# Kernel tuning notes

Hardware: AMD Instinct MI355X
Metric: run time of the kernel (lower is better)

The kernel has to match this reference:

```python
import jax, jax.numpy as jnp
import numpy as np

N, M = 2048, 256
INPUT_DIM, EMBED_DIM, HIDDEN = 512, 256, 512


def setup_inputs() -> dict:
    key = jax.random.key(0)
    ks = jax.random.split(key, 12)
    s = 0.02
    inp = {
        "x": jax.random.normal(ks[0], (N, INPUT_DIM), dtype=jnp.float32),
        "tuples": jax.random.randint(ks[1], (M, 3), 0, 8, dtype=jnp.int64),
        # x_net: Linear(input_dim, hidden) -> ReLU -> Linear(hidden, embed_dim) -> ReLU
        "Wa": s * jax.random.normal(ks[2], (HIDDEN, INPUT_DIM), dtype=jnp.float32),
        "ba": jnp.zeros((HIDDEN,), dtype=jnp.float32),
        "Wb": s * jax.random.normal(ks[3], (EMBED_DIM, HIDDEN), dtype=jnp.float32),
        "bb": jnp.zeros((EMBED_DIM,), dtype=jnp.float32),
        # embedding tables
        "E_pred": s * jax.random.normal(ks[4], (8, EMBED_DIM), dtype=jnp.float32),
        "E_filt": s * jax.random.normal(ks[5], (192, EMBED_DIM), dtype=jnp.float32),
        "E_reo": s * jax.random.normal(ks[6], (8, EMBED_DIM), dtype=jnp.float32),
        # mlp: Linear(2*embed_dim, hidden) -> ReLU -> Linear(hidden, 1)
        "W1": s * jax.random.normal(ks[7], (HIDDEN, 2 * EMBED_DIM), dtype=jnp.float32),
        "b1": jnp.zeros((HIDDEN,), dtype=jnp.float32),
        "W2": s * jax.random.normal(ks[8], (1, HIDDEN), dtype=jnp.float32),
        "b2": jnp.zeros((1,), dtype=jnp.float32),
    }
    return inp


def reference(x, tuples, Wa, ba, Wb, bb, E_pred, E_filt, E_reo, W1, b1, W2, b2):
    # x_net: two Linear+ReLU layers -> x_emb [N, D]
    h_x = jax.nn.relu(jnp.einsum('ni,hi->nh', x, Wa) + ba)
    x_emb = jax.nn.relu(jnp.einsum('nh,dh->nd', h_x, Wb) + bb)
    # tuple embedding sum -> t_emb [M, D]
    t_emb = E_pred[tuples[:, 0]] + E_filt[tuples[:, 1]] + E_reo[tuples[:, 2]]
    # mlp first layer on concat([x_exp, t_exp]) == Wx @ x_emb + Wt @ t_emb (split W1)
    D = x_emb.shape[1]
    W1x, W1t = W1[:, :D], W1[:, D:]
    hx = jnp.einsum('nd,hd->nh', x_emb, W1x)          # [N, H]
    ht = jnp.einsum('md,hd->mh', t_emb, W1t)          # [M, H]
    h = jax.nn.relu(hx[:, None, :] + ht[None, :, :] + b1)  # [N, M, H]
    out = jnp.einsum('nmh,h->nm', h, W2[0]) + b2[0]   # [N, M]
    return out
```

## Files before the change

kernel.cpp:

```cpp
#include <hip/hip_runtime.h>

constexpr int N_     = 2048;
constexpr int IN_DIM = 512;
constexpr int HID    = 512;
constexpr int EMB    = 256;
constexpr int M_     = 256;

typedef __attribute__((ext_vector_type(8))) short short8;
typedef __attribute__((ext_vector_type(4))) float f32x4;
typedef __attribute__((ext_vector_type(2))) _Float16 h2v;

union U32H2 { unsigned int u; h2v v; };

__device__ __forceinline__ unsigned short f2bf(float f) {
    union { float f; unsigned int u; } v; v.f = f;
    return (unsigned short)((v.u + 0x7fffu + ((v.u >> 16) & 1u)) >> 16);
}
__device__ __forceinline__ unsigned int packh2(float a, float b) {
    U32H2 r; r.v[0] = (_Float16)a; r.v[1] = (_Float16)b; return r.u;
}
__device__ __forceinline__ h2v relu2(h2v s) {
#if defined(__has_builtin) && __has_builtin(__builtin_elementwise_max)
    U32H2 z; z.u = 0u;
    return __builtin_elementwise_max(s, z.v);
#else
    U32H2 t; t.v = s;
    const unsigned int m = ((t.u & 0x80000000u) ? 0xFFFF0000u : 0u) |
                           ((t.u & 0x00008000u) ? 0x0000FFFFu : 0u);
    t.u &= ~m;
    return t.v;
#endif
}

__global__ __launch_bounds__(256)
void prep(const float* __restrict__ x, const float* __restrict__ Wa,
          const float* __restrict__ Wb, const float* __restrict__ W1,
          const int* __restrict__ tuples, const float* __restrict__ Ep,
          const float* __restrict__ Ef, const float* __restrict__ Er,
          const float* __restrict__ w2,
          unsigned short* __restrict__ x_bf, unsigned short* __restrict__ Wa_bf,
          unsigned short* __restrict__ Wb_bf, unsigned short* __restrict__ W1x_bf,
          unsigned short* __restrict__ W1t_bf, unsigned short* __restrict__ t_emb_bf,
          unsigned int* __restrict__ w2p)
{
    const int b = blockIdx.x, t = threadIdx.x;
    if (b < 1664) {
        int q = b * 256 + t;
        float4 v; ushort4 u;
        if (q < 262144) {
            v = ((const float4*)x)[q];
            u.x = f2bf(v.x); u.y = f2bf(v.y); u.z = f2bf(v.z); u.w = f2bf(v.w);
            ((ushort4*)x_bf)[q] = u;
        } else if ((q -= 262144) < 65536) {
            v = ((const float4*)Wa)[q];
            u.x = f2bf(v.x); u.y = f2bf(v.y); u.z = f2bf(v.z); u.w = f2bf(v.w);
            ((ushort4*)Wa_bf)[q] = u;
        } else if ((q -= 65536) < 32768) {
            v = ((const float4*)Wb)[q];
            u.x = f2bf(v.x); u.y = f2bf(v.y); u.z = f2bf(v.z); u.w = f2bf(v.w);
            ((ushort4*)Wb_bf)[q] = u;
        } else {
            q -= 32768;
            v = ((const float4*)W1)[q];
            u.x = f2bf(v.x); u.y = f2bf(v.y); u.z = f2bf(v.z); u.w = f2bf(v.w);
            const int row = q >> 7, c = (q & 127) * 4;
            if (c < 256) ((ushort4*)W1x_bf)[(row * 256 + c) >> 2] = u;
            else         ((ushort4*)W1t_bf)[(row * 256 + c - 256) >> 2] = u;
        }
    } else if (b < 1728) {
        const int idx = (b - 1664) * 256 + t;
        const int m = idx >> 6, q = idx & 63;
        const int t0 = tuples[m * 3 + 0];
        const int t1 = tuples[m * 3 + 1];
        const int t2 = tuples[m * 3 + 2];
        const float4 a = ((const float4*)(Ep + t0 * EMB))[q];
        const float4 c = ((const float4*)(Ef + t1 * EMB))[q];
        const float4 d = ((const float4*)(Er + t2 * EMB))[q];
        ushort4 u;
        u.x = f2bf(a.x + c.x + d.x);
        u.y = f2bf(a.y + c.y + d.y);
        u.z = f2bf(a.z + c.z + d.z);
        u.w = f2bf(a.w + c.w + d.w);
        ((ushort4*)t_emb_bf)[m * 64 + q] = u;
    } else {
        w2p[t] = packh2(w2[2 * t], w2[2 * t + 1]);
    }
}

template<int BM, int BN, bool RELU, bool BIASC>
__global__ __launch_bounds__(256)
void gemm_bf16(const unsigned short* __restrict__ A, int lda,
               const unsigned short* __restrict__ W, int ldw,
               const float* __restrict__ bias,
               unsigned short* __restrict__ Cout, int ldc, int K)
{
    constexpr int BK = 64;
    constexpr int SM = BM / 2, SN = BN / 2;
    constexpr int FM = SM / 16, FN = SN / 16;
    constexpr int AIT = BM / 32, WIT = BN / 32;
    __shared__ unsigned short As[BM][BK + 8];
    __shared__ unsigned short Bs[BN][BK + 8];

    const int tid  = threadIdx.x;
    const int row0 = blockIdx.x * BM, col0 = blockIdx.y * BN;
    const int wv = tid >> 6, lane = tid & 63;
    const int wr = wv >> 1, wc = wv & 1;
    const int lr = lane & 15, lq = lane >> 4;

    f32x4 acc[FM][FN];
#pragma unroll
    for (int i = 0; i < FM; ++i)
#pragma unroll
        for (int j = 0; j < FN; ++j) acc[i][j] = (f32x4)0.f;

    short8 pa[AIT], pw[WIT];
    auto issue = [&](int k0) {
#pragma unroll
        for (int i = 0; i < AIT; ++i) {
            const int idx = tid + i * 256, r = idx >> 3, c8 = idx & 7;
            pa[i] = *(const short8*)&A[(size_t)(row0 + r) * lda + k0 + c8 * 8];
        }
#pragma unroll
        for (int i = 0; i < WIT; ++i) {
            const int idx = tid + i * 256, r = idx >> 3, c8 = idx & 7;
            pw[i] = *(const short8*)&W[(size_t)(col0 + r) * ldw + k0 + c8 * 8];
        }
    };
    auto store = [&]() {
#pragma unroll
        for (int i = 0; i < AIT; ++i) {
            const int idx = tid + i * 256, r = idx >> 3, c8 = idx & 7;
            *(short8*)&As[r][c8 * 8] = pa[i];
        }
#pragma unroll
        for (int i = 0; i < WIT; ++i) {
            const int idx = tid + i * 256, r = idx >> 3, c8 = idx & 7;
            *(short8*)&Bs[r][c8 * 8] = pw[i];
        }
    };

    issue(0); store();
    const int NC = K / BK;
    for (int c = 0; c < NC; ++c) {
        if (c + 1 < NC) issue((c + 1) * BK);
        __syncthreads();
#pragma unroll
        for (int ks = 0; ks < 2; ++ks) {
            short8 af[FM], bfr[FN];
#pragma unroll
            for (int i = 0; i < FM; ++i)
                af[i] = *(const short8*)&As[wr * SM + i * 16 + lr][ks * 32 + lq * 8];
#pragma unroll
            for (int j = 0; j < FN; ++j)
                bfr[j] = *(const short8*)&Bs[wc * SN + j * 16 + lr][ks * 32 + lq * 8];
#pragma unroll
            for (int i = 0; i < FM; ++i)
#pragma unroll
                for (int j = 0; j < FN; ++j)
                    acc[i][j] = __builtin_amdgcn_mfma_f32_16x16x32_bf16(
                        af[i], bfr[j], acc[i][j], 0, 0, 0);
        }
        __syncthreads();
        if (c + 1 < NC) store();
    }

#pragma unroll
    for (int i = 0; i < FM; ++i) {
#pragma unroll
        for (int j = 0; j < FN; ++j) {
            const int colb = col0 + wc * SN + j * 16 + lr;
#pragma unroll
            for (int e = 0; e < 4; ++e) {
                const int row = row0 + wr * SM + i * 16 + lq * 4 + e;
                float v = acc[i][j][e];
                if (BIASC) v += bias[colb];
                if (RELU)  v = fmaxf(v, 0.f);
                Cout[(size_t)row * ldc + colb] = f2bf(v);
            }
        }
    }
}

__global__ __launch_bounds__(256)
void gemm_pair(const unsigned short* __restrict__ W1x_bf,
               const unsigned short* __restrict__ W1t_bf,
               const unsigned short* __restrict__ x_emb_bf,
               const unsigned short* __restrict__ t_emb_bf,
               const float* __restrict__ b1,
               unsigned int* __restrict__ hxT_p,
               unsigned int* __restrict__ cmT_p)
{
    constexpr int BM = 32, BN = 64, BK = 64;
    constexpr int SM = 16, SN = 32, FN = 2;
    __shared__ unsigned short As[BM][BK + 8];
    __shared__ unsigned short Bs[BN][BK + 8];

    const unsigned short* A; const unsigned short* B;
    const float* bias; unsigned int* outp; int ldc, col0;
    if (blockIdx.y < 32) {
        A = W1x_bf; B = x_emb_bf; bias = nullptr; outp = hxT_p;
        ldc = N_; col0 = blockIdx.y * BN;
    } else {
        A = W1t_bf; B = t_emb_bf; bias = b1; outp = cmT_p;
        ldc = M_; col0 = (blockIdx.y - 32) * BN;
    }
    const int K = EMB, row0 = blockIdx.x * BM;

    const int tid = threadIdx.x;
    const int wv = tid >> 6, lane = tid & 63;
    const int wr = wv >> 1, wc = wv & 1;
    const int lr = lane & 15, lq = lane >> 4;

    f32x4 acc[FN];
#pragma unroll
    for (int j = 0; j < FN; ++j) acc[j] = (f32x4)0.f;

    short8 pa, pw[2];
    auto issue = [&](int k0) {
        { const int r = tid >> 3, c8 = tid & 7;
          pa = *(const short8*)&A[(size_t)(row0 + r) * K + k0 + c8 * 8]; }
#pragma unroll
        for (int i = 0; i < 2; ++i) {
            const int idx = tid + i * 256, r = idx >> 3, c8 = idx & 7;
            pw[i] = *(const short8*)&B[(size_t)(col0 + r) * K + k0 + c8 * 8];
        }
    };
    auto store = [&]() {
        { const int r = tid >> 3, c8 = tid & 7;
          *(short8*)&As[r][c8 * 8] = pa; }
#pragma unroll
        for (int i = 0; i < 2; ++i) {
            const int idx = tid + i * 256, r = idx >> 3, c8 = idx & 7;
            *(short8*)&Bs[r][c8 * 8] = pw[i];
        }
    };

    issue(0); store();
    const int NC = K / BK;
    for (int c = 0; c < NC; ++c) {
        if (c + 1 < NC) issue((c + 1) * BK);
        __syncthreads();
#pragma unroll
        for (int ks = 0; ks < 2; ++ks) {
            short8 af, bfr[FN];
            af = *(const short8*)&As[wr * SM + lr][ks * 32 + lq * 8];
#pragma unroll
            for (int j = 0; j < FN; ++j)
                bfr[j] = *(const short8*)&Bs[wc * SN + j * 16 + lr][ks * 32 + lq * 8];
#pragma unroll
            for (int j = 0; j < FN; ++j)
                acc[j] = __builtin_amdgcn_mfma_f32_16x16x32_bf16(
                    af, bfr[j], acc[j], 0, 0, 0);
        }
        __syncthreads();
        if (c + 1 < NC) store();
    }

    const int rowb = row0 + wr * SM + lq * 4;
#pragma unroll
    for (int j = 0; j < FN; ++j) {
        const int colb = col0 + wc * SN + j * 16 + lr;
#pragma unroll
        for (int e2 = 0; e2 < 2; ++e2) {
            float v0 = acc[j][2 * e2], v1 = acc[j][2 * e2 + 1];
            if (bias) { v0 += bias[rowb + 2 * e2]; v1 += bias[rowb + 2 * e2 + 1]; }
            outp[(size_t)((rowb >> 1) + e2) * ldc + colb] = packh2(v0, v1);
        }
    }
}

__global__ __launch_bounds__(256, 4)
void fused_out(const unsigned int* __restrict__ hxT_p,
               const unsigned int* __restrict__ cmT_p,
               const unsigned int* __restrict__ w2p,
               unsigned int* __restrict__ part_u32)
{
    constexpr int TN = 64, TM = 32, H2B = 64;
    __shared__ unsigned int Hs[H2B][TN + 4];
    __shared__ unsigned int Cs[H2B][TM + 4];
    __shared__ unsigned int Wsh[H2B];

    const int tid = threadIdx.x;
    const int tx = tid & 15, ty = tid >> 4;
    const int n0 = blockIdx.x * TN;
    const int m0 = blockIdx.y * TM;
    const int z  = blockIdx.z;
    const int kb = z * H2B;

#pragma unroll
    for (int p = 0; p < 4; ++p) {
        const int idx = tid + p * 256, r = idx >> 4, c4 = idx & 15;
        *(uint4*)&Hs[r][c4 * 4] =
            *(const uint4*)&hxT_p[(size_t)(kb + r) * N_ + n0 + c4 * 4];
    }
#pragma unroll
    for (int p = 0; p < 2; ++p) {
        const int idx = tid + p * 256, r = idx >> 3, c4 = idx & 7;
        *(uint4*)&Cs[r][c4 * 4] =
            *(const uint4*)&cmT_p[(size_t)(kb + r) * M_ + m0 + c4 * 4];
    }
    if (tid < H2B) Wsh[tid] = w2p[kb + tid];
    __syncthreads();

    float accf[4][2];
    U32H2 facc[4][2];
#pragma unroll
    for (int i = 0; i < 4; ++i)
#pragma unroll
        for (int j = 0; j < 2; ++j) { accf[i][j] = 0.f; facc[i][j].u = 0u; }

#pragma unroll
    for (int hb = 0; hb < H2B / 8; ++hb) {
#pragma unroll
        for (int hh = 0; hh < 8; ++hh) {
            const int h = hb * 8 + hh;
            const uint4 av = *(const uint4*)&Hs[h][ty * 4];
            const uint2 bv = *(const uint2*)&Cs[h][tx * 2];
            U32H2 w; w.u = Wsh[h];
            U32H2 a[4], b[2];
            a[0].u = av.x; a[1].u = av.y; a[2].u = av.z; a[3].u = av.w;
            b[0].u = bv.x; b[1].u = bv.y;
#pragma unroll
            for (int i = 0; i < 4; ++i) {
#pragma unroll
                for (int j = 0; j < 2; ++j) {
                    const h2v s = relu2(a[i].v + b[j].v);
                    facc[i][j].v = s * w.v + facc[i][j].v;
                }
            }
        }
#pragma unroll
        for (int i = 0; i < 4; ++i)
#pragma unroll
            for (int j = 0; j < 2; ++j) {
                accf[i][j] += (float)facc[i][j].v[0] + (float)facc[i][j].v[1];
                facc[i][j].u = 0u;
            }
    }

#pragma unroll
    for (int i = 0; i < 4; ++i) {
        const int n = n0 + ty * 4 + i;
        part_u32[((size_t)z * N_ + n) * (M_ / 2) + (m0 >> 1) + tx] =
            packh2(accf[i][0], accf[i][1]);
    }
}

__global__ __launch_bounds__(256)
void reduce_out(const unsigned short* __restrict__ part,
                const float* __restrict__ b2,
                float* __restrict__ out)
{
    const int g = blockIdx.x * 256 + threadIdx.x;
    const int n = g >> 5;
    const int m0 = (g & 31) * 8;
    const float bb = b2[0];
    float s[8];
#pragma unroll
    for (int i = 0; i < 8; ++i) s[i] = bb;
#pragma unroll
    for (int zz = 0; zz < 4; ++zz) {
        const uint4 v = *(const uint4*)&part[((size_t)zz * N_ + n) * M_ + m0];
        const unsigned int vv[4] = {v.x, v.y, v.z, v.w};
#pragma unroll
        for (int q = 0; q < 4; ++q) {
            U32H2 u; u.u = vv[q];
            s[2 * q]     += (float)u.v[0];
            s[2 * q + 1] += (float)u.v[1];
        }
    }
    float4 o0 = {s[0], s[1], s[2], s[3]};
    float4 o1 = {s[4], s[5], s[6], s[7]};
    *(float4*)&out[(size_t)n * M_ + m0]     = o0;
    *(float4*)&out[(size_t)n * M_ + m0 + 4] = o1;
}

extern "C" void kernel_launch(void* const* d_in, const int* in_sizes, int n_in,
                              void* d_out, int out_size, void* d_ws, size_t ws_size,
                              hipStream_t stream)
{
    const float* x      = (const float*)d_in[0];
    const int*   tuples = (const int*)d_in[1];
    const float* Wa     = (const float*)d_in[2];
    const float* ba     = (const float*)d_in[3];
    const float* Wb     = (const float*)d_in[4];
    const float* bb     = (const float*)d_in[5];
    const float* E_pred = (const float*)d_in[6];
    const float* E_filt = (const float*)d_in[7];
    const float* E_reo  = (const float*)d_in[8];
    const float* W1     = (const float*)d_in[9];
    const float* b1     = (const float*)d_in[10];
    const float* W2     = (const float*)d_in[11];
    const float* b2     = (const float*)d_in[12];
    float* out = (float*)d_out;

    char* w = (char*)d_ws;
    unsigned short* x_bf     = (unsigned short*)(w + 0);
    unsigned int*   hxT_p    = (unsigned int*)(w + 0);
    unsigned short* h_x_bf   = (unsigned short*)(w + 2097152);
    unsigned int*   part_u32 = (unsigned int*)(w + 2097152);
    unsigned short* x_emb_bf = (unsigned short*)(w + 4194304);
    unsigned short* Wa_bf    = (unsigned short*)(w + 5242880);
    unsigned short* Wb_bf    = (unsigned short*)(w + 5767168);
    unsigned short* W1x_bf   = (unsigned short*)(w + 6029312);
    unsigned int*   cmT_p    = (unsigned int*)(w + 6291456);
    unsigned short* W1t_bf   = (unsigned short*)(w + 6553600);
    unsigned short* t_emb_bf = (unsigned short*)(w + 6815744);
    unsigned int*   w2p      = (unsigned int*)(w + 6946816);

    prep<<<dim3(1729), dim3(256), 0, stream>>>(
        x, Wa, Wb, W1, tuples, E_pred, E_filt, E_reo, W2,
        x_bf, Wa_bf, Wb_bf, W1x_bf, W1t_bf, t_emb_bf, w2p);

    gemm_bf16<32, 64, true, true><<<dim3(N_ / 32, HID / 64), 256, 0, stream>>>(
        x_bf, IN_DIM, Wa_bf, IN_DIM, ba, h_x_bf, HID, IN_DIM);

    gemm_bf16<32, 32, true, true><<<dim3(N_ / 32, EMB / 32), 256, 0, stream>>>(
        h_x_bf, HID, Wb_bf, HID, bb, x_emb_bf, EMB, HID);

    gemm_pair<<<dim3(HID / 32, 36), 256, 0, stream>>>(
        W1x_bf, W1t_bf, x_emb_bf, t_emb_bf, b1, hxT_p, cmT_p);

    fused_out<<<dim3(N_ / 64, M_ / 32, 4), 256, 0, stream>>>(
        hxT_p, cmT_p, w2p, part_u32);

    reduce_out<<<dim3(65536 / 256), 256, 0, stream>>>(
        (const unsigned short*)part_u32, b2, out);
}
```

Measured before the change: 120.8 us.

## Double-buffer GEMM shared tiles and widen fused_out tile with fdot2 accumulation

Both GEMM kernels now keep two shared-memory stages, so each iteration needs one barrier instead of two and the next tile can be stored while the current one is consumed. The fused_out kernel doubles its M tile to 64, so each thread computes a 4x4 output block. Where the fdot2 builtin is available, it accumulates the half2 relu products straight into fp32, replacing the packed-half FMA plus periodic conversion. The trade-offs are more registers and shared memory, a lower launch-bounds occupancy hint, and half as many fused_out blocks.

```diff
diff --git a/kernel.cpp b/kernel.cpp
--- a/kernel.cpp
+++ b/kernel.cpp
@@ -9,6 +9,12 @@
 typedef __attribute__((ext_vector_type(8))) short short8;
 typedef __attribute__((ext_vector_type(4))) float f32x4;
 typedef __attribute__((ext_vector_type(2))) _Float16 h2v;
+
+#if defined(__has_builtin)
+#if __has_builtin(__builtin_amdgcn_fdot2)
+#define HAVE_FDOT2 1
+#endif
+#endif
 
 union U32H2 { unsigned int u; h2v v; };
 
@@ -98,8 +104,8 @@
     constexpr int SM = BM / 2, SN = BN / 2;
     constexpr int FM = SM / 16, FN = SN / 16;
     constexpr int AIT = BM / 32, WIT = BN / 32;
-    __shared__ unsigned short As[BM][BK + 8];
-    __shared__ unsigned short Bs[BN][BK + 8];
+    __shared__ unsigned short As[2][BM][BK + 8];
+    __shared__ unsigned short Bs[2][BN][BK + 8];
 
     const int tid  = threadIdx.x;
     const int row0 = blockIdx.x * BM, col0 = blockIdx.y * BN;
@@ -126,33 +132,34 @@
             pw[i] = *(const short8*)&W[(size_t)(col0 + r) * ldw + k0 + c8 * 8];
         }
     };
-    auto store = [&]() {
+    auto store = [&](int bsel) {
 #pragma unroll
         for (int i = 0; i < AIT; ++i) {
             const int idx = tid + i * 256, r = idx >> 3, c8 = idx & 7;
-            *(short8*)&As[r][c8 * 8] = pa[i];
+            *(short8*)&As[bsel][r][c8 * 8] = pa[i];
         }
 #pragma unroll
         for (int i = 0; i < WIT; ++i) {
             const int idx = tid + i * 256, r = idx >> 3, c8 = idx & 7;
-            *(short8*)&Bs[r][c8 * 8] = pw[i];
+            *(short8*)&Bs[bsel][r][c8 * 8] = pw[i];
         }
     };
 
-    issue(0); store();
+    issue(0); store(0);
     const int NC = K / BK;
     for (int c = 0; c < NC; ++c) {
+        const int buf = c & 1;
+        __syncthreads();
         if (c + 1 < NC) issue((c + 1) * BK);
-        __syncthreads();
 #pragma unroll
         for (int ks = 0; ks < 2; ++ks) {
             short8 af[FM], bfr[FN];
 #pragma unroll
             for (int i = 0; i < FM; ++i)
-                af[i] = *(const short8*)&As[wr * SM + i * 16 + lr][ks * 32 + lq * 8];
+                af[i] = *(const short8*)&As[buf][wr * SM + i * 16 + lr][ks * 32 + lq * 8];
 #pragma unroll
             for (int j = 0; j < FN; ++j)
-                bfr[j] = *(const short8*)&Bs[wc * SN + j * 16 + lr][ks * 32 + lq * 8];
+                bfr[j] = *(const short8*)&Bs[buf][wc * SN + j * 16 + lr][ks * 32 + lq * 8];
 #pragma unroll
             for (int i = 0; i < FM; ++i)
 #pragma unroll
@@ -160,8 +167,7 @@
                     acc[i][j] = __builtin_amdgcn_mfma_f32_16x16x32_bf16(
                         af[i], bfr[j], acc[i][j], 0, 0, 0);
         }
-        __syncthreads();
-        if (c + 1 < NC) store();
+        if (c + 1 < NC) store((c + 1) & 1);
     }
 
 #pragma unroll
@@ -192,8 +198,8 @@
 {
     constexpr int BM = 32, BN = 64, BK = 64;
     constexpr int SM = 16, SN = 32, FN = 2;
-    __shared__ unsigned short As[BM][BK + 8];
-    __shared__ unsigned short Bs[BN][BK + 8];
+    __shared__ unsigned short As[2][BM][BK + 8];
+    __shared__ unsigned short Bs[2][BN][BK + 8];
 
     const unsigned short* A; const unsigned short* B;
     const float* bias; unsigned int* outp; int ldc, col0;
@@ -225,35 +231,35 @@
             pw[i] = *(const short8*)&B[(size_t)(col0 + r) * K + k0 + c8 * 8];
         }
     };
-    auto store = [&]() {
+    auto store = [&](int bsel) {
         { const int r = tid >> 3, c8 = tid & 7;
-          *(short8*)&As[r][c8 * 8] = pa; }
+          *(short8*)&As[bsel][r][c8 * 8] = pa; }
 #pragma unroll
         for (int i = 0; i < 2; ++i) {
             const int idx = tid + i * 256, r = idx >> 3, c8 = idx & 7;
-            *(short8*)&Bs[r][c8 * 8] = pw[i];
+            *(short8*)&Bs[bsel][r][c8 * 8] = pw[i];
         }
     };
 
-    issue(0); store();
+    issue(0); store(0);
     const int NC = K / BK;
     for (int c = 0; c < NC; ++c) {
+        const int buf = c & 1;
+        __syncthreads();
         if (c + 1 < NC) issue((c + 1) * BK);
-        __syncthreads();
 #pragma unroll
         for (int ks = 0; ks < 2; ++ks) {
             short8 af, bfr[FN];
-            af = *(const short8*)&As[wr * SM + lr][ks * 32 + lq * 8];
+            af = *(const short8*)&As[buf][wr * SM + lr][ks * 32 + lq * 8];
 #pragma unroll
             for (int j = 0; j < FN; ++j)
-                bfr[j] = *(const short8*)&Bs[wc * SN + j * 16 + lr][ks * 32 + lq * 8];
+                bfr[j] = *(const short8*)&Bs[buf][wc * SN + j * 16 + lr][ks * 32 + lq * 8];
 #pragma unroll
             for (int j = 0; j < FN; ++j)
                 acc[j] = __builtin_amdgcn_mfma_f32_16x16x32_bf16(
                     af, bfr[j], acc[j], 0, 0, 0);
         }
-        __syncthreads();
-        if (c + 1 < NC) store();
+        if (c + 1 < NC) store((c + 1) & 1);
     }
 
     const int rowb = row0 + wr * SM + lq * 4;
@@ -269,13 +275,13 @@
     }
 }
 
-__global__ __launch_bounds__(256, 4)
+__global__ __launch_bounds__(256, 2)
 void fused_out(const unsigned int* __restrict__ hxT_p,
                const unsigned int* __restrict__ cmT_p,
                const unsigned int* __restrict__ w2p,
                unsigned int* __restrict__ part_u32)
 {
-    constexpr int TN = 64, TM = 32, H2B = 64;
+    constexpr int TN = 64, TM = 64, H2B = 64;
     __shared__ unsigned int Hs[H2B][TN + 4];
     __shared__ unsigned int Cs[H2B][TM + 4];
     __shared__ unsigned int Wsh[H2B];
@@ -284,65 +290,83 @@
     const int tx = tid & 15, ty = tid >> 4;
     const int n0 = blockIdx.x * TN;
     const int m0 = blockIdx.y * TM;
-    const int z  = blockIdx.z;
-    const int kb = z * H2B;
+    const int kb = blockIdx.z * H2B;
 
 #pragma unroll
     for (int p = 0; p < 4; ++p) {
         const int idx = tid + p * 256, r = idx >> 4, c4 = idx & 15;
         *(uint4*)&Hs[r][c4 * 4] =
             *(const uint4*)&hxT_p[(size_t)(kb + r) * N_ + n0 + c4 * 4];
-    }
-#pragma unroll
-    for (int p = 0; p < 2; ++p) {
-        const int idx = tid + p * 256, r = idx >> 3, c4 = idx & 7;
         *(uint4*)&Cs[r][c4 * 4] =
             *(const uint4*)&cmT_p[(size_t)(kb + r) * M_ + m0 + c4 * 4];
     }
     if (tid < H2B) Wsh[tid] = w2p[kb + tid];
     __syncthreads();
 
-    float accf[4][2];
-    U32H2 facc[4][2];
+    float acc[4][4];
 #pragma unroll
     for (int i = 0; i < 4; ++i)
 #pragma unroll
-        for (int j = 0; j < 2; ++j) { accf[i][j] = 0.f; facc[i][j].u = 0u; }
-
+        for (int j = 0; j < 4; ++j) acc[i][j] = 0.f;
+
+#ifdef HAVE_FDOT2
+#pragma unroll 8
+    for (int h = 0; h < H2B; ++h) {
+        const uint4 av = *(const uint4*)&Hs[h][ty * 4];
+        const uint4 bv = *(const uint4*)&Cs[h][tx * 4];
+        U32H2 w; w.u = Wsh[h];
+        U32H2 a[4], b[4];
+        a[0].u = av.x; a[1].u = av.y; a[2].u = av.z; a[3].u = av.w;
+        b[0].u = bv.x; b[1].u = bv.y; b[2].u = bv.z; b[3].u = bv.w;
+#pragma unroll
+        for (int i = 0; i < 4; ++i)
+#pragma unroll
+            for (int j = 0; j < 4; ++j) {
+                const h2v s = relu2(a[i].v + b[j].v);
+                acc[i][j] = __builtin_amdgcn_fdot2(s, w.v, acc[i][j], false);
+            }
+    }
+#else
+    U32H2 facc[4][4];
+#pragma unroll
+    for (int i = 0; i < 4; ++i)
+#pragma unroll
+        for (int j = 0; j < 4; ++j) facc[i][j].u = 0u;
 #pragma unroll
     for (int hb = 0; hb < H2B / 8; ++hb) {
 #pragma unroll
         for (int hh = 0; hh < 8; ++hh) {
             const int h = hb * 8 + hh;
             const uint4 av = *(const uint4*)&Hs[h][ty * 4];
-            const uint2 bv = *(const uint2*)&Cs[h][tx * 2];
+            const uint4 bv = *(const uint4*)&Cs[h][tx * 4];
             U32H2 w; w.u = Wsh[h];
-            U32H2 a[4], b[2];
+            U32H2 a[4], b[4];
             a[0].u = av.x; a[1].u = av.y; a[2].u = av.z; a[3].u = av.w;
-            b[0].u = bv.x; b[1].u = bv.y;
-#pragma unroll
-            for (int i = 0; i < 4; ++i) {
-#pragma unroll
-                for (int j = 0; j < 2; ++j) {
+            b[0].u = bv.x; b[1].u = bv.y; b[2].u = bv.z; b[3].u = bv.w;
+#pragma unroll
+            for (int i = 0; i < 4; ++i)
+#pragma unroll
+                for (int j = 0; j < 4; ++j) {
                     const h2v s = relu2(a[i].v + b[j].v);
                     facc[i][j].v = s * w.v + facc[i][j].v;
                 }
-            }
         }
 #pragma unroll
         for (int i = 0; i < 4; ++i)
 #pragma unroll
-            for (int j = 0; j < 2; ++j) {
-                accf[i][j] += (float)facc[i][j].v[0] + (float)facc[i][j].v[1];
+            for (int j = 0; j < 4; ++j) {
+                acc[i][j] += (float)facc[i][j].v[0] + (float)facc[i][j].v[1];
                 facc[i][j].u = 0u;
             }
     }
+#endif
 
 #pragma unroll
     for (int i = 0; i < 4; ++i) {
         const int n = n0 + ty * 4 + i;
-        part_u32[((size_t)z * N_ + n) * (M_ / 2) + (m0 >> 1) + tx] =
-            packh2(accf[i][0], accf[i][1]);
+        const size_t base = ((size_t)blockIdx.z * N_ + n) * (M_ / 2) + (m0 >> 1) + tx * 2;
+        part_u32[base]     = packh2(acc[i][0], acc[i][1]);
+        part_u32[base + 1] = packh2(acc[i][2], acc[i][3]);
     }
 }
 
@@ -421,7 +445,7 @@
     gemm_pair<<<dim3(HID / 32, 36), 256, 0, stream>>>(
         W1x_bf, W1t_bf, x_emb_bf, t_emb_bf, b1, hxT_p, cmT_p);
 
-    fused_out<<<dim3(N_ / 64, M_ / 32, 4), 256, 0, stream>>>(
+    fused_out<<<dim3(N_ / 64, M_ / 64, 4), 256, 0, stream>>>(
         hxT_p, cmT_p, w2p, part_u32);
 
     reduce_out<<<dim3(65536 / 256), 256, 0, stream>>>(
```

New measurement: 121.1 us. Within noise of the previous version (+0.2%).
